# Optimization experiments

Measured on AMD Instinct MI355X. Metric: run time of the kernel, lower is better.

## Reference

```python
import jax, jax.numpy as jnp
import numpy as np

B, N, E, H, FF = 8, 1024, 512, 8, 2048
D = E // H
SCALE = D ** -0.5
EPS = 1e-5


def _layernorm(x, g, b):
    mu = jnp.mean(x, axis=-1, keepdims=True)
    var = jnp.mean((x - mu) ** 2, axis=-1, keepdims=True)
    return (x - mu) * jax.lax.rsqrt(var + EPS) * g + b


def setup_inputs() -> dict:
    key = jax.random.key(0)
    ks = jax.random.split(key, 16)
    s = lambda fan_in: 1.0 / np.sqrt(fan_in)
    inp = {"x": jax.random.normal(ks[0], (B, N, E), jnp.float32)}
    # attention projections, stored as [in, out] so y = x @ W + b
    inp["Wq"] = jax.random.uniform(ks[1], (E, E), jnp.float32, -s(E), s(E))
    inp["bq"] = jnp.zeros((E,), jnp.float32)
    inp["Wk"] = jax.random.uniform(ks[2], (E, E), jnp.float32, -s(E), s(E))
    inp["bk"] = jnp.zeros((E,), jnp.float32)
    inp["Wv"] = jax.random.uniform(ks[3], (E, E), jnp.float32, -s(E), s(E))
    inp["bv"] = jnp.zeros((E,), jnp.float32)
    inp["Wo"] = jax.random.uniform(ks[4], (E, E), jnp.float32, -s(E), s(E))
    inp["bo"] = jnp.zeros((E,), jnp.float32)
    # layernorms
    inp["g1"] = jnp.ones((E,), jnp.float32)
    inp["b1"] = jnp.zeros((E,), jnp.float32)
    inp["g2"] = jnp.ones((E,), jnp.float32)
    inp["b2"] = jnp.zeros((E,), jnp.float32)
    # feed-forward
    inp["W1"] = jax.random.uniform(ks[5], (E, FF), jnp.float32, -s(E), s(E))
    inp["bf1"] = jnp.zeros((FF,), jnp.float32)
    inp["W2"] = jax.random.uniform(ks[6], (FF, E), jnp.float32, -s(FF), s(FF))
    inp["bf2"] = jnp.zeros((E,), jnp.float32)
    return inp


def reference(x, Wq, bq, Wk, bk, Wv, bv, Wo, bo, g1, b1, g2, b2, W1, bf1, W2, bf2):
    # --- multi-head self-attention (equivalent to the edge scatter-softmax:
    # softmax over all source nodes j for each target node i) ---
    q = (x @ Wq + bq).reshape(B, N, H, D)
    k = (x @ Wk + bk).reshape(B, N, H, D)
    v = (x @ Wv + bv).reshape(B, N, H, D)
    scores = jnp.einsum("bnhd,bmhd->bhnm", q, k) * SCALE  # [B,H,N,N]
    attn = jax.nn.softmax(scores, axis=-1)
    ctx = jnp.einsum("bhnm,bmhd->bnhd", attn, v).reshape(B, N, E)
    attn_out = ctx @ Wo + bo
    # --- residual + norm1 ---
    h1 = _layernorm(x + attn_out, g1, b1)
    # --- FFN: linear -> relu -> linear ---
    ffn = jax.nn.relu(h1 @ W1 + bf1) @ W2 + bf2
    # --- residual + norm2 ---
    return _layernorm(h1 + ffn, g2, b2)
```

## Files before the change

### kernel.cpp

```cpp
#include <hip/hip_runtime.h>
#include <cstdint>
#include <cstddef>

typedef unsigned short u16;
typedef __attribute__((ext_vector_type(8))) short bf16x8;
typedef __attribute__((ext_vector_type(4))) float f32x4;
typedef __attribute__((ext_vector_type(16))) float f32x16;

#define EPI_F32 0
#define EPI_BF16_RELU 1
#define EPI_QKV 2
#define EPI_PART 3

#define QSCALE 0.18033688011112042f

__device__ __forceinline__ u16 f2bf(float f) {
  uint32_t u = __float_as_uint(f);
  return (u16)((u + 0x7FFFu + ((u >> 16) & 1u)) >> 16);
}

__device__ __forceinline__ uint32_t cvt_pk_bf16(float lo, float hi) {
  uint32_t r;
  asm("v_cvt_pk_bf16_f32 %0, %1, %2" : "=v"(r) : "v"(lo), "v"(hi));
  return r;
}

__device__ __forceinline__ float fexp2(float x) { return __builtin_amdgcn_exp2f(x); }

__device__ __forceinline__ void gload_lds16(const void* g, void* l) {
  __builtin_amdgcn_global_load_lds((const __attribute__((address_space(1))) void*)g,
                                   (__attribute__((address_space(3))) void*)l, 16, 0, 0);
}

__global__ __launch_bounds__(256) void cvt_kernel(const float* __restrict__ in,
                                                  u16* __restrict__ out, int n8) {
  const int i = blockIdx.x * 256 + threadIdx.x;
  if (i >= n8) return;
  const float4* p = (const float4*)in + (size_t)i * 2;
  float4 a = p[0], b = p[1];
  union { u16 u[8]; uint4 q; } pk;
  pk.u[0] = f2bf(a.x); pk.u[1] = f2bf(a.y); pk.u[2] = f2bf(a.z); pk.u[3] = f2bf(a.w);
  pk.u[4] = f2bf(b.x); pk.u[5] = f2bf(b.y); pk.u[6] = f2bf(b.z); pk.u[7] = f2bf(b.w);
  ((uint4*)out)[i] = pk.q;
}

__global__ __launch_bounds__(256) void tcvt_kernel(const float* __restrict__ W,
                                                   u16* __restrict__ Wt, int K, int N) {
  __shared__ float tl[32][33];
  const int t = threadIdx.x;
  const int kr0 = blockIdx.y * 32, nc0 = blockIdx.x * 32;
  const int r = t >> 3, cq = (t & 7) * 4;
  float4 v = *(const float4*)&W[(size_t)(kr0 + r) * N + nc0 + cq];
  tl[r][cq + 0] = v.x; tl[r][cq + 1] = v.y; tl[r][cq + 2] = v.z; tl[r][cq + 3] = v.w;
  __syncthreads();
  union { u16 u[4]; uint2 q; } pk;
#pragma unroll
  for (int j = 0; j < 4; ++j) pk.u[j] = f2bf(tl[cq + j][r]);
  *(uint2*)&Wt[(size_t)(nc0 + r) * K + kr0 + cq] = pk.q;
}

__global__ __launch_bounds__(256) void tcvt4_kernel(
    const float* __restrict__ Wq, const float* __restrict__ Wk,
    const float* __restrict__ Wv, const float* __restrict__ Wo,
    u16* __restrict__ outQKV, u16* __restrict__ outO) {
  __shared__ float tl[32][33];
  const int z = blockIdx.z;
  const float* W = z == 0 ? Wq : (z == 1 ? Wk : (z == 2 ? Wv : Wo));
  u16* Wt = z < 3 ? outQKV + z * 262144 : outO;
  const int t = threadIdx.x;
  const int kr0 = blockIdx.y * 32, nc0 = blockIdx.x * 32;
  const int r = t >> 3, cq = (t & 7) * 4;
  float4 v = *(const float4*)&W[(size_t)(kr0 + r) * 512 + nc0 + cq];
  tl[r][cq + 0] = v.x; tl[r][cq + 1] = v.y; tl[r][cq + 2] = v.z; tl[r][cq + 3] = v.w;
  __syncthreads();
  union { u16 u[4]; uint2 q; } pk;
#pragma unroll
  for (int j = 0; j < 4; ++j) pk.u[j] = f2bf(tl[cq + j][r]);
  *(uint2*)&Wt[(size_t)(nc0 + r) * 512 + kr0 + cq] = pk.q;
}

__global__ __launch_bounds__(256) void packb_kernel(const float* __restrict__ bq,
                                                    const float* __restrict__ bk,
                                                    const float* __restrict__ bv,
                                                    float* __restrict__ out) {
  const int i = blockIdx.x * 256 + threadIdx.x;
  if (i >= 1536) return;
  out[i] = i < 512 ? bq[i] : (i < 1024 ? bk[i - 512] : bv[i - 1024]);
}

template<int BM, int BN, int WM, int WN, int EPI, int SPLIT>
__global__ __launch_bounds__(256) void gemm_kernel(
    const u16* __restrict__ A, const u16* __restrict__ Bt,
    const float* __restrict__ bias, void* __restrict__ out,
    int M, int N, int K) {
  constexpr int NWN = BN / WN;
  constexpr int MI = WM / 16, NI = WN / 16;
  __shared__ u16 As[BM * 32];
  __shared__ u16 Bs[BN * 32];
  const int tid = threadIdx.x;
  const int lane = tid & 63;
  const int wave = tid >> 6;
  const int m0 = blockIdx.y * BM;
  const int n0 = blockIdx.x * BN;
  const int wm = wave / NWN, wn = wave % NWN;
  const int g = lane >> 4, lr = lane & 15;
  const int srow = lane >> 2, scol = (lane & 3) * 8;

  f32x4 acc[MI][NI] = {};

  const int kBeg = (SPLIT > 1) ? blockIdx.z * (K / SPLIT) : 0;
  const int kEnd = (SPLIT > 1) ? kBeg + (K / SPLIT) : K;
  for (int k0 = kBeg; k0 < kEnd; k0 += 32) {
#pragma unroll
    for (int ch = wave; ch < BM / 16; ch += 4)
      gload_lds16(A + (size_t)(m0 + ch * 16 + srow) * K + k0 + scol, &As[ch * 512]);
#pragma unroll
    for (int ch = wave; ch < BN / 16; ch += 4)
      gload_lds16(Bt + (size_t)(n0 + ch * 16 + srow) * K + k0 + scol, &Bs[ch * 512]);
    __syncthreads();
    bf16x8 a[MI], b[NI];
#pragma unroll
    for (int mi = 0; mi < MI; ++mi) a[mi] = *(const bf16x8*)&As[(wm * WM + mi * 16 + lr) * 32 + g * 8];
#pragma unroll
    for (int ni = 0; ni < NI; ++ni) b[ni] = *(const bf16x8*)&Bs[(wn * WN + ni * 16 + lr) * 32 + g * 8];
#pragma unroll
    for (int mi = 0; mi < MI; ++mi)
#pragma unroll
      for (int ni = 0; ni < NI; ++ni)
        acc[mi][ni] = __builtin_amdgcn_mfma_f32_16x16x32_bf16(a[mi], b[ni], acc[mi][ni], 0, 0, 0);
    __syncthreads();
  }

#pragma unroll
  for (int mi = 0; mi < MI; ++mi) {
#pragma unroll
    for (int ni = 0; ni < NI; ++ni) {
      const int col = n0 + wn * WN + ni * 16 + lr;
      const float bv = (EPI == EPI_PART) ? 0.f : bias[col];
      f32x4 v = acc[mi][ni];
#pragma unroll
      for (int r = 0; r < 4; ++r) {
        const int row = m0 + wm * WM + mi * 16 + g * 4 + r;
        const float y = v[r] + bv;
        if (EPI == EPI_F32) {
          ((float*)out)[(size_t)row * N + col] = y;
        } else if (EPI == EPI_PART) {
          ((float*)out)[(size_t)blockIdx.z * M * N + (size_t)row * N + col] = y;
        } else if (EPI == EPI_BF16_RELU) {
          ((u16*)out)[(size_t)row * N + col] = f2bf(fmaxf(y, 0.f));
        } else {
          u16* qb = (u16*)out;
          const int sec = col >> 9, cs = col & 511;
          const int b = row >> 10, t = row & 1023, h = cs >> 6, d = cs & 63;
          if (sec == 0)
            qb[((size_t)((b * 8 + h) * 1024 + t)) * 64 + d] = f2bf(y * QSCALE);
          else if (sec == 1)
            qb[4194304 + ((size_t)((b * 8 + h) * 1024 + t)) * 64 + d] = f2bf(y);
          else
            qb[8388608 + ((size_t)((b * 8 + h) * 64 + d)) * 1024 + t] = f2bf(y);
        }
      }
    }
  }
}

__global__ __launch_bounds__(256, 2) void attn4_kernel(
    const u16* __restrict__ Q, const u16* __restrict__ K,
    const u16* __restrict__ Vt, u16* __restrict__ ctx) {
  __shared__ u16 smem[16384];
  const int tid = threadIdx.x, lane = tid & 63, w = tid >> 6;
  const int bh = blockIdx.x >> 3, qb = blockIdx.x & 7;
  const int c = lane & 31, g = lane >> 5;
  const int q0 = qb * 128 + w * 32;

  const u16* Qp = Q + ((size_t)bh * 1024 + q0 + c) * 64 + g * 8;
  const bf16x8 qf0 = *(const bf16x8*)(Qp);
  const bf16x8 qf1 = *(const bf16x8*)(Qp + 16);
  const bf16x8 qf2 = *(const bf16x8*)(Qp + 32);
  const bf16x8 qf3 = *(const bf16x8*)(Qp + 48);

  const u16* Kbase = K + (size_t)bh * 65536;
  const u16* Vbase = Vt + (size_t)bh * 65536;

  const int r0 = w * 16 + (lane >> 3), r1 = r0 + 8;
  const int cg0 = ((lane & 7) ^ (r0 & 7)) << 3;
  const int cg1 = ((lane & 7) ^ (r1 & 7)) << 3;

#define STAGE(buf, key0) do {                                                       \
    gload_lds16(Kbase + (size_t)((key0) + r0) * 64 + cg0, &smem[(buf)*4096 + w*1024]);       \
    gload_lds16(Kbase + (size_t)((key0) + r1) * 64 + cg1, &smem[(buf)*4096 + w*1024 + 512]); \
    gload_lds16(Vbase + (size_t)r0 * 1024 + (key0) + cg0, &smem[8192 + (buf)*4096 + w*1024]);\
    gload_lds16(Vbase + (size_t)r1 * 1024 + (key0) + cg1, &smem[8192 + (buf)*4096 + w*1024 + 512]); \
  } while (0)

  const int cs = c & 7;
  const int ro0 = c * 64, ro1 = (32 + c) * 64;
#define KS(buf, ro, cg) (*(const bf16x8*)&smem[(buf)*4096 + (ro) + ((((cg)) ^ cs) << 3)])
#define VS(buf, ro, cg) (*(const bf16x8*)&smem[8192 + (buf)*4096 + (ro) + ((((cg)) ^ cs) << 3)])

  f32x16 cacc[2] = {};
  float mrun = -1e30f, lrun = 0.f;

  STAGE(0, 0);
  __syncthreads();

  for (int kt = 0; kt < 16; ++kt) {
    const int buf = kt & 1;
    if (kt < 15) STAGE(buf ^ 1, (kt + 1) * 64);

    const bf16x8 kf0 = KS(buf, ro0, g),     kf1 = KS(buf, ro0, 2 + g);
    const bf16x8 kf2 = KS(buf, ro0, 4 + g), kf3 = KS(buf, ro0, 6 + g);
    const bf16x8 kf4 = KS(buf, ro1, g),     kf5 = KS(buf, ro1, 2 + g);
    const bf16x8 kf6 = KS(buf, ro1, 4 + g), kf7 = KS(buf, ro1, 6 + g);

    f32x16 sa = {}, sb = {};
    sa = __builtin_amdgcn_mfma_f32_32x32x16_bf16(kf0, qf0, sa, 0, 0, 0);
    sb = __builtin_amdgcn_mfma_f32_32x32x16_bf16(kf4, qf0, sb, 0, 0, 0);
    sa = __builtin_amdgcn_mfma_f32_32x32x16_bf16(kf1, qf1, sa, 0, 0, 0);
    sb = __builtin_amdgcn_mfma_f32_32x32x16_bf16(kf5, qf1, sb, 0, 0, 0);
    sa = __builtin_amdgcn_mfma_f32_32x32x16_bf16(kf2, qf2, sa, 0, 0, 0);
    sb = __builtin_amdgcn_mfma_f32_32x32x16_bf16(kf6, qf2, sb, 0, 0, 0);
    sa = __builtin_amdgcn_mfma_f32_32x32x16_bf16(kf3, qf3, sa, 0, 0, 0);
    sb = __builtin_amdgcn_mfma_f32_32x32x16_bf16(kf7, qf3, sb, 0, 0, 0);

    float tm[16];
#pragma unroll
    for (int r = 0; r < 16; ++r) tm[r] = fmaxf(sa[r], sb[r]);
#pragma unroll
    for (int st = 8; st >= 1; st >>= 1)
#pragma unroll
      for (int r = 0; r < st; ++r) tm[r] = fmaxf(tm[r], tm[r + st]);
    const float mt = fmaxf(tm[0], __shfl_xor(tm[0], 32));
    if (!__all(mt <= mrun)) {
      const float mnew = fmaxf(mrun, mt);
      const float al = fexp2(mrun - mnew);
#pragma unroll
      for (int r = 0; r < 16; ++r) { cacc[0][r] *= al; cacc[1][r] *= al; }
      lrun *= al;
      mrun = mnew;
    }
    float pa[16], pb[16];
#pragma unroll
    for (int r = 0; r < 16; ++r) pa[r] = fexp2(sa[r] - mrun);
#pragma unroll
    for (int r = 0; r < 16; ++r) pb[r] = fexp2(sb[r] - mrun);
    float ts[16];
#pragma unroll
    for (int r = 0; r < 16; ++r) ts[r] = pa[r] + pb[r];
#pragma unroll
    for (int st = 8; st >= 1; st >>= 1)
#pragma unroll
      for (int r = 0; r < st; ++r) ts[r] += ts[r + st];
    lrun += ts[0] + __shfl_xor(ts[0], 32);

    uint32_t wda[8], pwa[8], wdb[8], pwb[8];
#pragma unroll
    for (int i = 0; i < 8; ++i) wda[i] = cvt_pk_bf16(pa[2 * i], pa[2 * i + 1]);
#pragma unroll
    for (int i = 0; i < 8; ++i) wdb[i] = cvt_pk_bf16(pb[2 * i], pb[2 * i + 1]);
#pragma unroll
    for (int i = 0; i < 8; ++i) pwa[i] = __shfl_xor((int)wda[i], 32);
#pragma unroll
    for (int i = 0; i < 8; ++i) pwb[i] = __shfl_xor((int)wdb[i], 32);
    union { uint32_t u[4]; bf16x8 v; } b0a, b1a, b0b, b1b;
    const bool glo = (g == 0);
    b0a.u[0] = glo ? wda[0] : pwa[2]; b0a.u[1] = glo ? wda[1] : pwa[3];
    b0a.u[2] = glo ? pwa[0] : wda[2]; b0a.u[3] = glo ? pwa[1] : wda[3];
    b1a.u[0] = glo ? wda[4] : pwa[6]; b1a.u[1] = glo ? wda[5] : pwa[7];
    b1a.u[2] = glo ? pwa[4] : wda[6]; b1a.u[3] = glo ? pwa[5] : wda[7];
    b0b.u[0] = glo ? wdb[0] : pwb[2]; b0b.u[1] = glo ? wdb[1] : pwb[3];
    b0b.u[2] = glo ? pwb[0] : wdb[2]; b0b.u[3] = glo ? pwb[1] : wdb[3];
    b1b.u[0] = glo ? wdb[4] : pwb[6]; b1b.u[1] = glo ? wdb[5] : pwb[7];
    b1b.u[2] = glo ? pwb[4] : wdb[6]; b1b.u[3] = glo ? pwb[5] : wdb[7];

    const bf16x8 va00 = VS(buf, ro0, g),     va01 = VS(buf, ro0, 2 + g);
    const bf16x8 vb00 = VS(buf, ro0, 4 + g), vb01 = VS(buf, ro0, 6 + g);
    const bf16x8 va10 = VS(buf, ro1, g),     va11 = VS(buf, ro1, 2 + g);
    const bf16x8 vb10 = VS(buf, ro1, 4 + g), vb11 = VS(buf, ro1, 6 + g);

    cacc[0] = __builtin_amdgcn_mfma_f32_32x32x16_bf16(va00, b0a.v, cacc[0], 0, 0, 0);
    cacc[1] = __builtin_amdgcn_mfma_f32_32x32x16_bf16(va10, b0a.v, cacc[1], 0, 0, 0);
    cacc[0] = __builtin_amdgcn_mfma_f32_32x32x16_bf16(va01, b1a.v, cacc[0], 0, 0, 0);
    cacc[1] = __builtin_amdgcn_mfma_f32_32x32x16_bf16(va11, b1a.v, cacc[1], 0, 0, 0);
    cacc[0] = __builtin_amdgcn_mfma_f32_32x32x16_bf16(vb00, b0b.v, cacc[0], 0, 0, 0);
    cacc[1] = __builtin_amdgcn_mfma_f32_32x32x16_bf16(vb10, b0b.v, cacc[1], 0, 0, 0);
    cacc[0] = __builtin_amdgcn_mfma_f32_32x32x16_bf16(vb01, b1b.v, cacc[0], 0, 0, 0);
    cacc[1] = __builtin_amdgcn_mfma_f32_32x32x16_bf16(vb11, b1b.v, cacc[1], 0, 0, 0);

    __syncthreads();
  }

  const float inv = 1.0f / lrun;
  u16* tw = &smem[w * 2048];
#pragma unroll
  for (int h2 = 0; h2 < 2; ++h2) {
#pragma unroll
    for (int rq = 0; rq < 4; ++rq) {
      const u16 x0 = f2bf(cacc[h2][4 * rq + 0] * inv);
      const u16 x1 = f2bf(cacc[h2][4 * rq + 1] * inv);
      const u16 x2 = f2bf(cacc[h2][4 * rq + 2] * inv);
      const u16 x3 = f2bf(cacc[h2][4 * rq + 3] * inv);
      uint2 val;
      val.x = (uint32_t)x0 | ((uint32_t)x1 << 16);
      val.y = (uint32_t)x2 | ((uint32_t)x3 << 16);
      const int chunk = h2 * 4 + rq;
      *(uint2*)&tw[c * 64 + ((chunk ^ (c & 7)) * 8) + 4 * g] = val;
    }
  }
  __syncthreads();
  const int b_ = bh >> 3, h_ = bh & 7;
#pragma unroll
  for (int t = 0; t < 4; ++t) {
    const int lcg = t * 256 + tid;
    const int wv = lcg >> 8, rem = lcg & 255;
    const int q = rem >> 3, cg = rem & 7;
    const uint4 val = *(const uint4*)&smem[wv * 2048 + q * 64 + ((cg ^ (q & 7)) * 8)];
    const int grow = qb * 128 + wv * 32 + q;
    *(uint4*)&ctx[((size_t)(b_ * 1024 + grow)) * 512 + h_ * 64 + cg * 8] = val;
  }
#undef STAGE
#undef KS
#undef VS
}

template<bool ABF16>
__global__ __launch_bounds__(256) void lnc_kernel(
    const void* __restrict__ Av, const float* __restrict__ P0,
    const float* __restrict__ P1, const float* __restrict__ pb,
    const float* __restrict__ gw, const float* __restrict__ bw,
    float* __restrict__ outF, u16* __restrict__ outB) {
  const int lane = threadIdx.x & 63, wave = threadIdx.x >> 6;
  const int row = blockIdx.x * 4 + wave;
  float a[8];
  if (ABF16) {
    const uint4 q = ((const uint4*)((const u16*)Av + (size_t)row * 512))[lane];
    const u16* pu = (const u16*)&q;
#pragma unroll
    for (int j = 0; j < 8; ++j) a[j] = __uint_as_float((uint32_t)pu[j] << 16);
  } else {
    const float4* a4 = (const float4*)((const float*)Av + (size_t)row * 512);
    const float4 x0 = a4[lane * 2], x1 = a4[lane * 2 + 1];
    a[0] = x0.x; a[1] = x0.y; a[2] = x0.z; a[3] = x0.w;
    a[4] = x1.x; a[5] = x1.y; a[6] = x1.z; a[7] = x1.w;
  }
  const float4* p04 = (const float4*)(P0 + (size_t)row * 512);
  const float4* p14 = (const float4*)(P1 + (size_t)row * 512);
  const float4 q00 = p04[lane * 2], q01 = p04[lane * 2 + 1];
  const float4 q10 = p14[lane * 2], q11 = p14[lane * 2 + 1];
  const float4 e0 = ((const float4*)pb)[lane * 2], e1 = ((const float4*)pb)[lane * 2 + 1];
  float v[8] = {a[0] + q00.x + q10.x + e0.x, a[1] + q00.y + q10.y + e0.y,
                a[2] + q00.z + q10.z + e0.z, a[3] + q00.w + q10.w + e0.w,
                a[4] + q01.x + q11.x + e1.x, a[5] + q01.y + q11.y + e1.y,
                a[6] + q01.z + q11.z + e1.z, a[7] + q01.w + q11.w + e1.w};
  float s = 0.f;
#pragma unroll
  for (int j = 0; j < 8; ++j) s += v[j];
#pragma unroll
  for (int off = 32; off >= 1; off >>= 1) s += __shfl_xor(s, off);
  const float mu = s * (1.f / 512.f);
  float vs = 0.f;
#pragma unroll
  for (int j = 0; j < 8; ++j) { const float d = v[j] - mu; vs += d * d; }
#pragma unroll
  for (int off = 32; off >= 1; off >>= 1) vs += __shfl_xor(vs, off);
  const float rstd = rsqrtf(vs * (1.f / 512.f) + 1e-5f);
  const float4 gA = ((const float4*)gw)[lane * 2], gB = ((const float4*)gw)[lane * 2 + 1];
  const float4 bA = ((const float4*)bw)[lane * 2], bB = ((const float4*)bw)[lane * 2 + 1];
  const float og[8] = {gA.x, gA.y, gA.z, gA.w, gB.x, gB.y, gB.z, gB.w};
  const float ob[8] = {bA.x, bA.y, bA.z, bA.w, bB.x, bB.y, bB.z, bB.w};
  float o[8];
#pragma unroll
  for (int j = 0; j < 8; ++j) o[j] = (v[j] - mu) * rstd * og[j] + ob[j];
  if (outF) {
    float4 w0 = {o[0], o[1], o[2], o[3]}, w1 = {o[4], o[5], o[6], o[7]};
    ((float4*)(outF + (size_t)row * 512))[lane * 2] = w0;
    ((float4*)(outF + (size_t)row * 512))[lane * 2 + 1] = w1;
  }
  if (outB) {
    union { u16 u[8]; uint4 q; } pk;
#pragma unroll
    for (int j = 0; j < 8; ++j) pk.u[j] = f2bf(o[j]);
    ((uint4*)(outB + (size_t)row * 512))[lane] = pk.q;
  }
}

extern "C" void kernel_launch(void* const* d_in, const int* in_sizes, int n_in,
                              void* d_out, int out_size, void* d_ws, size_t ws_size,
                              hipStream_t stream) {
  const float* x   = (const float*)d_in[0];
  const float* Wq  = (const float*)d_in[1];
  const float* bq  = (const float*)d_in[2];
  const float* Wk  = (const float*)d_in[3];
  const float* bk  = (const float*)d_in[4];
  const float* Wv  = (const float*)d_in[5];
  const float* bv  = (const float*)d_in[6];
  const float* Wo  = (const float*)d_in[7];
  const float* bo  = (const float*)d_in[8];
  const float* g1  = (const float*)d_in[9];
  const float* b1  = (const float*)d_in[10];
  const float* g2  = (const float*)d_in[11];
  const float* b2  = (const float*)d_in[12];
  const float* W1  = (const float*)d_in[13];
  const float* bf1 = (const float*)d_in[14];
  const float* W2  = (const float*)d_in[15];
  const float* bf2 = (const float*)d_in[16];

  char* ws = (char*)d_ws;
  u16*   xb    = (u16*)(ws + 0);
  u16*   Wqkvt = (u16*)(ws + 8388608);
  u16*   Wot   = (u16*)(ws + 9961472);
  u16*   W1t   = (u16*)(ws + 10485760);
  u16*   W2t   = (u16*)(ws + 12582912);
  u16*   Qb    = (u16*)(ws + 14680064);
  u16*   ctx   = (u16*)(ws + 39845888);
  float* P0    = (float*)(ws + 48234496);
  u16*   h1b   = (u16*)(ws + 81788928);
  u16*   mid   = (u16*)(ws + 14680064);
  float* bqkv  = (float*)(ws + 39845888);

  cvt_kernel<<<2048, 256, 0, stream>>>(x, xb, 524288);
  tcvt4_kernel<<<dim3(16, 16, 4), 256, 0, stream>>>(Wq, Wk, Wv, Wo, Wqkvt, Wot);
  tcvt_kernel<<<dim3(64, 16), 256, 0, stream>>>(W1, W1t, 512, 2048);
  tcvt_kernel<<<dim3(16, 64), 256, 0, stream>>>(W2, W2t, 2048, 512);
  packb_kernel<<<6, 256, 0, stream>>>(bq, bk, bv, bqkv);

  gemm_kernel<128, 128, 64, 64, EPI_QKV, 1><<<dim3(12, 64), 256, 0, stream>>>(
      xb, Wqkvt, bqkv, Qb, 8192, 1536, 512);

  attn4_kernel<<<512, 256, 0, stream>>>(Qb, Qb + 4194304, Qb + 8388608, ctx);

  gemm_kernel<64, 128, 64, 32, EPI_PART, 2><<<dim3(4, 128, 2), 256, 0, stream>>>(
      ctx, Wot, nullptr, P0, 8192, 512, 512);
  lnc_kernel<false><<<2048, 256, 0, stream>>>(x, P0, P0 + 4194304, bo, g1, b1,
                                              nullptr, h1b);

  gemm_kernel<128, 128, 64, 64, EPI_BF16_RELU, 1><<<dim3(16, 64), 256, 0, stream>>>(
      h1b, W1t, bf1, mid, 8192, 2048, 512);

  gemm_kernel<64, 128, 64, 32, EPI_PART, 2><<<dim3(4, 128, 2), 256, 0, stream>>>(
      mid, W2t, nullptr, P0, 8192, 512, 2048);
  lnc_kernel<true><<<2048, 256, 0, stream>>>(h1b, P0, P0 + 4194304, bf2, g2, b2,
                                             (float*)d_out, nullptr);
}
```

Before: 270.2 us.

## Add double-buffered swizzled GEMM, fuse prep launches, use bf16 residual in LN1

Adds gemm2_kernel, which stages 64-wide K tiles into two LDS buffers with direct global-to-LDS loads and an XOR swizzle. It overlaps the next tile's loads with MFMA work and is used for the QKV and FFN1 GEMMs. The five separate conversion and packing kernels are merged into one prep_kernel launch to cut launch overhead. The first layernorm now reads the bf16 copy of x as its residual instead of fp32 x, which reduces memory traffic but lowers residual precision slightly.

```diff
diff --git a/kernel.cpp b/kernel.cpp
--- a/kernel.cpp
+++ b/kernel.cpp
@@ -32,23 +32,10 @@
                                    (__attribute__((address_space(3))) void*)l, 16, 0, 0);
 }
 
-__global__ __launch_bounds__(256) void cvt_kernel(const float* __restrict__ in,
-                                                  u16* __restrict__ out, int n8) {
-  const int i = blockIdx.x * 256 + threadIdx.x;
-  if (i >= n8) return;
-  const float4* p = (const float4*)in + (size_t)i * 2;
-  float4 a = p[0], b = p[1];
-  union { u16 u[8]; uint4 q; } pk;
-  pk.u[0] = f2bf(a.x); pk.u[1] = f2bf(a.y); pk.u[2] = f2bf(a.z); pk.u[3] = f2bf(a.w);
-  pk.u[4] = f2bf(b.x); pk.u[5] = f2bf(b.y); pk.u[6] = f2bf(b.z); pk.u[7] = f2bf(b.w);
-  ((uint4*)out)[i] = pk.q;
-}
-
-__global__ __launch_bounds__(256) void tcvt_kernel(const float* __restrict__ W,
-                                                   u16* __restrict__ Wt, int K, int N) {
-  __shared__ float tl[32][33];
-  const int t = threadIdx.x;
-  const int kr0 = blockIdx.y * 32, nc0 = blockIdx.x * 32;
+__device__ __forceinline__ void tcvt_tile(const float* __restrict__ W,
+                                          u16* __restrict__ Wt, int K, int N,
+                                          int bx, int by, float (*tl)[33], int t) {
+  const int kr0 = by * 32, nc0 = bx * 32;
   const int r = t >> 3, cq = (t & 7) * 4;
   float4 v = *(const float4*)&W[(size_t)(kr0 + r) * N + nc0 + cq];
   tl[r][cq + 0] = v.x; tl[r][cq + 1] = v.y; tl[r][cq + 2] = v.z; tl[r][cq + 3] = v.w;
@@ -59,33 +46,154 @@
   *(uint2*)&Wt[(size_t)(nc0 + r) * K + kr0 + cq] = pk.q;
 }
 
-__global__ __launch_bounds__(256) void tcvt4_kernel(
+__global__ __launch_bounds__(256) void prep_kernel(
+    const float* __restrict__ x, u16* __restrict__ xb,
     const float* __restrict__ Wq, const float* __restrict__ Wk,
     const float* __restrict__ Wv, const float* __restrict__ Wo,
-    u16* __restrict__ outQKV, u16* __restrict__ outO) {
+    u16* __restrict__ Wqkvt, u16* __restrict__ Wot,
+    const float* __restrict__ W1, u16* __restrict__ W1t,
+    const float* __restrict__ W2, u16* __restrict__ W2t,
+    const float* __restrict__ bq, const float* __restrict__ bk,
+    const float* __restrict__ bv, float* __restrict__ bqkv) {
   __shared__ float tl[32][33];
-  const int z = blockIdx.z;
-  const float* W = z == 0 ? Wq : (z == 1 ? Wk : (z == 2 ? Wv : Wo));
-  u16* Wt = z < 3 ? outQKV + z * 262144 : outO;
-  const int t = threadIdx.x;
-  const int kr0 = blockIdx.y * 32, nc0 = blockIdx.x * 32;
-  const int r = t >> 3, cq = (t & 7) * 4;
-  float4 v = *(const float4*)&W[(size_t)(kr0 + r) * 512 + nc0 + cq];
-  tl[r][cq + 0] = v.x; tl[r][cq + 1] = v.y; tl[r][cq + 2] = v.z; tl[r][cq + 3] = v.w;
-  __syncthreads();
-  union { u16 u[4]; uint2 q; } pk;
-#pragma unroll
-  for (int j = 0; j < 4; ++j) pk.u[j] = f2bf(tl[cq + j][r]);
-  *(uint2*)&Wt[(size_t)(nc0 + r) * 512 + kr0 + cq] = pk.q;
-}
-
-__global__ __launch_bounds__(256) void packb_kernel(const float* __restrict__ bq,
-                                                    const float* __restrict__ bk,
-                                                    const float* __restrict__ bv,
-                                                    float* __restrict__ out) {
-  const int i = blockIdx.x * 256 + threadIdx.x;
-  if (i >= 1536) return;
-  out[i] = i < 512 ? bq[i] : (i < 1024 ? bk[i - 512] : bv[i - 1024]);
+  const int b = blockIdx.x, t = threadIdx.x;
+  if (b < 2048) {
+    const int i = b * 256 + t;
+    const float4* p = (const float4*)x + (size_t)i * 2;
+    float4 a = p[0], c = p[1];
+    union { u16 u[8]; uint4 q; } pk;
+    pk.u[0] = f2bf(a.x); pk.u[1] = f2bf(a.y); pk.u[2] = f2bf(a.z); pk.u[3] = f2bf(a.w);
+    pk.u[4] = f2bf(c.x); pk.u[5] = f2bf(c.y); pk.u[6] = f2bf(c.z); pk.u[7] = f2bf(c.w);
+    ((uint4*)xb)[i] = pk.q;
+  } else if (b < 3072) {
+    const int u = b - 2048, z = u >> 8, s = u & 255;
+    const float* W = z == 0 ? Wq : (z == 1 ? Wk : (z == 2 ? Wv : Wo));
+    u16* Wt = z < 3 ? Wqkvt + z * 262144 : Wot;
+    tcvt_tile(W, Wt, 512, 512, s & 15, s >> 4, tl, t);
+  } else if (b < 4096) {
+    const int u = b - 3072;
+    tcvt_tile(W1, W1t, 512, 2048, u % 64, u / 64, tl, t);
+  } else if (b < 5120) {
+    const int u = b - 4096;
+    tcvt_tile(W2, W2t, 2048, 512, u % 16, u / 16, tl, t);
+  } else {
+    const int i = (b - 5120) * 256 + t;
+    if (i < 1536) bqkv[i] = i < 512 ? bq[i] : (i < 1024 ? bk[i - 512] : bv[i - 1024]);
+  }
+}
+
+template<int BM, int BN, int WM, int WN, int EPI, int SPLIT>
+__global__ __launch_bounds__(256, 2) void gemm2_kernel(
+    const u16* __restrict__ A, const u16* __restrict__ Bt,
+    const float* __restrict__ bias, void* __restrict__ out,
+    int M, int N, int K) {
+  constexpr int NWN = BN / WN;
+  constexpr int MI = WM / 16, NI = WN / 16;
+  __shared__ u16 As[2][BM * 64];
+  __shared__ u16 Bs[2][BN * 64];
+  const int tid = threadIdx.x, lane = tid & 63, wave = tid >> 6;
+  const int m0 = blockIdx.y * BM, n0 = blockIdx.x * BN;
+  const int wm = wave / NWN, wn = wave % NWN;
+  const int g = lane >> 4, lr = lane & 15;
+  const int srow = tid >> 3, sslot = tid & 7;
+
+#define STAGE2(buf, k0) do {                                                        \
+    _Pragma("unroll")                                                               \
+    for (int i_ = 0; i_ < BM / 32; ++i_) {                                          \
+      const int r_ = i_ * 32 + srow;                                                \
+      gload_lds16(A + (size_t)(m0 + r_) * K + (k0) + ((sslot ^ (r_ & 7)) << 3),     \
+                  &As[buf][i_ * 2048 + tid * 8]);                                   \
+    }                                                                               \
+    _Pragma("unroll")                                                               \
+    for (int i_ = 0; i_ < BN / 32; ++i_) {                                          \
+      const int r_ = i_ * 32 + srow;                                                \
+      gload_lds16(Bt + (size_t)(n0 + r_) * K + (k0) + ((sslot ^ (r_ & 7)) << 3),    \
+                  &Bs[buf][i_ * 2048 + tid * 8]);                                   \
+    }                                                                               \
+  } while (0)
+
+  f32x4 acc[MI][NI] = {};
+  const int kBeg = (SPLIT > 1) ? blockIdx.z * (K / SPLIT) : 0;
+  const int NT = ((SPLIT > 1) ? K / SPLIT : K) >> 6;
+
+  STAGE2(0, kBeg);
+  STAGE2(1, kBeg + 64);
+  asm volatile("s_waitcnt vmcnt(8)" ::: "memory");
+  __builtin_amdgcn_s_barrier();
+  asm volatile("" ::: "memory");
+
+  for (int t = 0; t < NT; ++t) {
+    const int cur = t & 1;
+    bf16x8 af[MI][2], bf[NI][2];
+#pragma unroll
+    for (int step = 0; step < 2; ++step) {
+#pragma unroll
+      for (int mi = 0; mi < MI; ++mi) {
+        const int r = wm * WM + mi * 16 + lr;
+        af[mi][step] = *(const bf16x8*)&As[cur][r * 64 + ((((step << 2) + g) ^ (r & 7)) << 3)];
+      }
+#pragma unroll
+      for (int ni = 0; ni < NI; ++ni) {
+        const int r = wn * WN + ni * 16 + lr;
+        bf[ni][step] = *(const bf16x8*)&Bs[cur][r * 64 + ((((step << 2) + g) ^ (r & 7)) << 3)];
+      }
+    }
+    __builtin_amdgcn_s_setprio(1);
+#pragma unroll
+    for (int step = 0; step < 2; ++step)
+#pragma unroll
+      for (int mi = 0; mi < MI; ++mi)
+#pragma unroll
+        for (int ni = 0; ni < NI; ++ni)
+          acc[mi][ni] = __builtin_amdgcn_mfma_f32_16x16x32_bf16(af[mi][step], bf[ni][step],
+                                                                acc[mi][ni], 0, 0, 0);
+    __builtin_amdgcn_s_setprio(0);
+    asm volatile("s_waitcnt lgkmcnt(0)" ::: "memory");
+    __builtin_amdgcn_sched_barrier(0);
+    __builtin_amdgcn_s_barrier();
+    asm volatile("" ::: "memory");
+    if (t + 2 < NT) {
+      STAGE2(cur, kBeg + (t + 2) * 64);
+      asm volatile("s_waitcnt vmcnt(8)" ::: "memory");
+    } else {
+      asm volatile("s_waitcnt vmcnt(0)" ::: "memory");
+    }
+    __builtin_amdgcn_s_barrier();
+    asm volatile("" ::: "memory");
+  }
+#undef STAGE2
+
+#pragma unroll
+  for (int mi = 0; mi < MI; ++mi) {
+#pragma unroll
+    for (int ni = 0; ni < NI; ++ni) {
+      const int col = n0 + wn * WN + ni * 16 + lr;
+      const float bv = (EPI == EPI_PART) ? 0.f : bias[col];
+      f32x4 v = acc[mi][ni];
+#pragma unroll
+      for (int r = 0; r < 4; ++r) {
+        const int row = m0 + wm * WM + mi * 16 + g * 4 + r;
+        const float y = v[r] + bv;
+        if (EPI == EPI_F32) {
+          ((float*)out)[(size_t)row * N + col] = y;
+        } else if (EPI == EPI_PART) {
+          ((float*)out)[(size_t)blockIdx.z * M * N + (size_t)row * N + col] = y;
+        } else if (EPI == EPI_BF16_RELU) {
+          ((u16*)out)[(size_t)row * N + col] = f2bf(fmaxf(y, 0.f));
+        } else {
+          u16* qb = (u16*)out;
+          const int sec = col >> 9, cs = col & 511;
+          const int b = row >> 10, tt = row & 1023, h = cs >> 6, d = cs & 63;
+          if (sec == 0)
+            qb[((size_t)((b * 8 + h) * 1024 + tt)) * 64 + d] = f2bf(y * QSCALE);
+          else if (sec == 1)
+            qb[4194304 + ((size_t)((b * 8 + h) * 1024 + tt)) * 64 + d] = f2bf(y);
+          else
+            qb[8388608 + ((size_t)((b * 8 + h) * 64 + d)) * 1024 + tt] = f2bf(y);
+        }
+      }
+    }
+  }
 }
 
 template<int BM, int BN, int WM, int WN, int EPI, int SPLIT>
@@ -148,16 +256,6 @@
           ((float*)out)[(size_t)blockIdx.z * M * N + (size_t)row * N + col] = y;
         } else if (EPI == EPI_BF16_RELU) {
           ((u16*)out)[(size_t)row * N + col] = f2bf(fmaxf(y, 0.f));
-        } else {
-          u16* qb = (u16*)out;
-          const int sec = col >> 9, cs = col & 511;
-          const int b = row >> 10, t = row & 1023, h = cs >> 6, d = cs & 63;
-          if (sec == 0)
-            qb[((size_t)((b * 8 + h) * 1024 + t)) * 64 + d] = f2bf(y * QSCALE);
-          else if (sec == 1)
-            qb[4194304 + ((size_t)((b * 8 + h) * 1024 + t)) * 64 + d] = f2bf(y);
-          else
-            qb[8388608 + ((size_t)((b * 8 + h) * 64 + d)) * 1024 + t] = f2bf(y);
         }
       }
     }
@@ -418,23 +516,20 @@
   u16*   mid   = (u16*)(ws + 14680064);
   float* bqkv  = (float*)(ws + 39845888);
 
-  cvt_kernel<<<2048, 256, 0, stream>>>(x, xb, 524288);
-  tcvt4_kernel<<<dim3(16, 16, 4), 256, 0, stream>>>(Wq, Wk, Wv, Wo, Wqkvt, Wot);
-  tcvt_kernel<<<dim3(64, 16), 256, 0, stream>>>(W1, W1t, 512, 2048);
-  tcvt_kernel<<<dim3(16, 64), 256, 0, stream>>>(W2, W2t, 2048, 512);
-  packb_kernel<<<6, 256, 0, stream>>>(bq, bk, bv, bqkv);
-
-  gemm_kernel<128, 128, 64, 64, EPI_QKV, 1><<<dim3(12, 64), 256, 0, stream>>>(
+  prep_kernel<<<5126, 256, 0, stream>>>(x, xb, Wq, Wk, Wv, Wo, Wqkvt, Wot,
+                                        W1, W1t, W2, W2t, bq, bk, bv, bqkv);
+
+  gemm2_kernel<128, 128, 64, 64, EPI_QKV, 1><<<dim3(12, 64), 256, 0, stream>>>(
       xb, Wqkvt, bqkv, Qb, 8192, 1536, 512);
 
   attn4_kernel<<<512, 256, 0, stream>>>(Qb, Qb + 4194304, Qb + 8388608, ctx);
 
   gemm_kernel<64, 128, 64, 32, EPI_PART, 2><<<dim3(4, 128, 2), 256, 0, stream>>>(
       ctx, Wot, nullptr, P0, 8192, 512, 512);
-  lnc_kernel<false><<<2048, 256, 0, stream>>>(x, P0, P0 + 4194304, bo, g1, b1,
-                                              nullptr, h1b);
-
-  gemm_kernel<128, 128, 64, 64, EPI_BF16_RELU, 1><<<dim3(16, 64), 256, 0, stream>>>(
+  lnc_kernel<true><<<2048, 256, 0, stream>>>(xb, P0, P0 + 4194304, bo, g1, b1,
+                                             nullptr, h1b);
+
+  gemm2_kernel<128, 128, 64, 64, EPI_BF16_RELU, 1><<<dim3(16, 64), 256, 0, stream>>>(
       h1b, W1t, bf1, mid, 8192, 2048, 512);
 
   gemm_kernel<64, 128, 64, 32, EPI_PART, 2><<<dim3(4, 128, 2), 256, 0, stream>>>(
```

Result: faster. 264.6 us (-2.1%).
